# Optimization experiments

Measured on AMD Instinct MI355X. Metric: run time of the kernel, lower is better.

## Reference

```python
import math
import jax, jax.numpy as jnp
import numpy as np

HIDDEN = 1024
INTER = 2048
NUM_EXPERTS = 8          # includes 1 noop slot (last column)
TOP_K = 2
CAPACITY_FACTOR = 1.0
BATCH, SEQ = 4, 4096


def setup_inputs() -> dict:
    key = jax.random.key(0)
    k_x, k_rw, k_ei, k_eo = jax.random.split(key, 4)
    x = jax.random.normal(k_x, (BATCH, SEQ, HIDDEN), dtype=jnp.float32)
    # Router: nn.Linear(hidden, num_experts) with xavier_uniform weight, zero-ish bias
    limit = math.sqrt(6.0 / (HIDDEN + NUM_EXPERTS))
    router_w = jax.random.uniform(k_rw, (NUM_EXPERTS, HIDDEN), dtype=jnp.float32,
                                  minval=-limit, maxval=limit)
    router_b = jnp.zeros((NUM_EXPERTS,), dtype=jnp.float32)
    # Expert params initialized with randn, exactly as in the torch module
    experts_inter = jax.random.normal(k_ei, (NUM_EXPERTS - 1, HIDDEN, INTER), dtype=jnp.float32)
    experts_out = jax.random.normal(k_eo, (NUM_EXPERTS - 1, INTER, HIDDEN), dtype=jnp.float32)
    return {"x": x, "router_w": router_w, "router_b": router_b,
            "experts_inter": experts_inter, "experts_out": experts_out}


def reference(x, router_w, router_b, experts_inter, experts_out):
    B, S, H = x.shape
    E = router_w.shape[0]
    N = B * S
    capacity = math.ceil(N / E * CAPACITY_FACTOR)  # static (shapes are static)

    x_flat = x.reshape(N, H)
    # Router: linear + softmax over experts
    weights = jax.nn.softmax(x_flat @ router_w.T + router_b, axis=-1)   # [N, E]

    # Top-k sparsification: keep top-k weights per token, zero the rest
    vals, idx = jax.lax.top_k(weights, TOP_K)                            # [N, k]
    topk_w = jnp.zeros_like(weights).at[jnp.arange(N)[:, None], idx].set(vals)

    # Last expert column is the no-op (identity) path
    noop_routed = x_flat * topk_w[:, -1:]                                # [N, H]

    expert_w = topk_w[:, :-1]                                            # [N, E-1]
    mask = (expert_w > 0).astype(jnp.int32)                              # [N, E-1]

    # Per-expert: sort tokens by routing mask (descending), take first `capacity`
    sorted_idx = jnp.argsort(-mask, axis=0)[:capacity]                   # [C, E-1], stable
    sorted_mask = jnp.take_along_axis(mask, sorted_idx, axis=0)          # [C, E-1]

    used_idx = (sorted_idx * sorted_mask).reshape(-1)                    # [C*(E-1)]
    toks = x_flat[used_idx] * sorted_mask.reshape(-1)[:, None].astype(x.dtype)
    toks = toks.reshape(capacity, E - 1, H)                              # [C, E-1, H]
    in_w = jnp.take_along_axis(expert_w, sorted_idx, axis=0)             # [C, E-1]

    # Grouped expert FFN: relu(x W1) W2, weighted by routing prob
    h = jax.nn.relu(jnp.einsum('ceh,ehi->cei', toks, experts_inter))     # [C, E-1, I]
    out = jnp.einsum('cei,eih->ceh', h, experts_out) * in_w[..., None]   # [C, E-1, H]

    # Scatter-add combine (masked slots contribute zeros at index 0)
    combined = jnp.zeros_like(x_flat).at[used_idx].add(out.reshape(-1, H))
    combined = combined + noop_routed
    return combined.reshape(B, S, H)
```

## Files before the change

### kernel.cpp

```cpp
#include <hip/hip_runtime.h>
#include <stdint.h>

#define HIDDEN 1024
#define INTER 2048
#define NEXP 8
#define NE 7
#define NTOK 16384
#define CAP 2048
#define BM 64
#define BN 64
#define BK 64
#define GBM 128
#define GBN 128

typedef __attribute__((ext_vector_type(8))) short short8;
typedef __attribute__((ext_vector_type(4))) float f32x4;

__device__ __forceinline__ unsigned short f2bf(float f) {
  union { float f; unsigned int u; } v;
  v.f = f;
  unsigned int u = v.u;
  unsigned int r = (u + 0x7FFFu + ((u >> 16) & 1u)) >> 16;
  return (unsigned short)r;
}

typedef __attribute__((address_space(1))) const unsigned int gu32;
typedef __attribute__((address_space(3))) unsigned int lu32;
__device__ __forceinline__ void gload16(const void* g, void* l) {
  __builtin_amdgcn_global_load_lds((gu32*)g, (lu32*)l, 16, 0, 0);
}

__global__ __launch_bounds__(256) void prologue_kernel(
    const float* __restrict__ x, const float* __restrict__ rw,
    const float* __restrict__ rb, float* __restrict__ expw,
    float* __restrict__ noopw, unsigned short* __restrict__ xbf,
    float* __restrict__ out) {
  if (blockIdx.x == NTOK / 4) {
    unsigned int* z = (unsigned int*)(xbf + (size_t)NTOK * HIDDEN);
    z[threadIdx.x] = 0u;
    z[threadIdx.x + 256] = 0u;
    return;
  }
  int wid = threadIdx.x >> 6;
  int lane = threadIdx.x & 63;
  int token = blockIdx.x * 4 + wid;
  const float* xr = x + (size_t)token * HIDDEN;
  float4 xv[4];
  float acc[NEXP];
#pragma unroll
  for (int e = 0; e < NEXP; e++) acc[e] = 0.f;
#pragma unroll
  for (int j = 0; j < 4; j++) {
    xv[j] = *(const float4*)(xr + j * 256 + lane * 4);
#pragma unroll
    for (int e = 0; e < NEXP; e++) {
      float4 wv = *(const float4*)(rw + e * HIDDEN + j * 256 + lane * 4);
      acc[e] = fmaf(xv[j].x, wv.x, acc[e]);
      acc[e] = fmaf(xv[j].y, wv.y, acc[e]);
      acc[e] = fmaf(xv[j].z, wv.z, acc[e]);
      acc[e] = fmaf(xv[j].w, wv.w, acc[e]);
    }
  }
#pragma unroll
  for (int e = 0; e < NEXP; e++) {
    float a = acc[e];
#pragma unroll
    for (int off = 32; off > 0; off >>= 1) a += __shfl_xor(a, off);
    acc[e] = a + rb[e];
  }
  float nwv = 0.f;
  if (lane == 0) {
    float m = acc[0];
#pragma unroll
    for (int e = 1; e < NEXP; e++) m = fmaxf(m, acc[e]);
    float w[NEXP];
    float s = 0.f;
#pragma unroll
    for (int e = 0; e < NEXP; e++) { w[e] = expf(acc[e] - m); s += w[e]; }
    float inv = 1.f / s;
#pragma unroll
    for (int e = 0; e < NEXP; e++) w[e] *= inv;
    int t1 = 0;
#pragma unroll
    for (int e = 1; e < NEXP; e++) if (w[e] > w[t1]) t1 = e;
    int t2 = (t1 == 0) ? 1 : 0;
#pragma unroll
    for (int e = 0; e < NEXP; e++) if (e != t1 && w[e] > w[t2]) t2 = e;
    nwv = (t1 == NEXP - 1) ? w[t1] : ((t2 == NEXP - 1) ? w[t2] : 0.f);
    noopw[token] = nwv;
#pragma unroll
    for (int e = 0; e < NE; e++) {
      float v = 0.f;
      if (e == t1) v = w[e];
      if (e == t2) v = w[e];
      expw[(size_t)e * NTOK + token] = v;
    }
  }
  float nw = __shfl(nwv, 0);
  float* orow = out + (size_t)token * HIDDEN;
  unsigned short* brow = xbf + (size_t)token * HIDDEN;
#pragma unroll
  for (int j = 0; j < 4; j++) {
    float4 o = xv[j];
    o.x *= nw; o.y *= nw; o.z *= nw; o.w *= nw;
    *(float4*)(orow + j * 256 + lane * 4) = o;
    ushort4 b;
    b.x = f2bf(xv[j].x); b.y = f2bf(xv[j].y);
    b.z = f2bf(xv[j].z); b.w = f2bf(xv[j].w);
    *(ushort4*)(brow + j * 256 + lane * 4) = b;
  }
}

__global__ __launch_bounds__(1024) void assign_par_kernel(
    const float* __restrict__ expw, int* __restrict__ slot_tok,
    float* __restrict__ slot_w) {
  int e = blockIdx.x;
  int tid = threadIdx.x;
  int lane = tid & 63, w = tid >> 6;
  __shared__ int wtot[16];
  const float* we = expw + (size_t)e * NTOK;
  int base = 0;
#pragma unroll 1
  for (int r = 0; r < NTOK / 1024; r++) {
    int t = r * 1024 + tid;
    float wv = we[t];
    bool flag = wv > 0.f;
    unsigned long long mask = __ballot(flag);
    int lp = __popcll(mask & ((1ull << lane) - 1ull));
    if (lane == 0) wtot[w] = __popcll(mask);
    __syncthreads();
    int pre = 0, tot = 0;
#pragma unroll
    for (int i = 0; i < 16; i++) {
      int v = wtot[i];
      pre += (i < w) ? v : 0;
      tot += v;
    }
    int pos = base + pre + lp;
    if (flag && pos < CAP) {
      slot_tok[e * CAP + pos] = t;
      slot_w[e * CAP + pos] = wv;
    }
    base += tot;
    __syncthreads();
    if (base >= CAP) break;
  }
  int cnt = base < CAP ? base : CAP;
  for (int p = cnt + tid; p < CAP; p += 1024) {
    slot_tok[e * CAP + p] = -1;
    slot_w[e * CAP + p] = 0.f;
  }
}

__global__ __launch_bounds__(256) void transpose_bf16_kernel(
    const float* __restrict__ in, unsigned short* __restrict__ outp,
    int K, int N) {
  int e = blockIdx.z;
  const float* src = in + (size_t)e * K * N;
  unsigned short* dst = outp + (size_t)e * K * N;
  int k0 = blockIdx.y * 64;
  int n0 = blockIdx.x * 64;
  __shared__ float tile[64][65];
  int tid = threadIdx.x;
  int nr = tid & 15;
  int kr = tid >> 4;
#pragma unroll
  for (int i = 0; i < 4; i++) {
    int k = i * 16 + kr;
    float4 v = *(const float4*)(src + (size_t)(k0 + k) * N + n0 + nr * 4);
    tile[k][nr * 4 + 0] = v.x;
    tile[k][nr * 4 + 1] = v.y;
    tile[k][nr * 4 + 2] = v.z;
    tile[k][nr * 4 + 3] = v.w;
  }
  __syncthreads();
  int g = tid & 7;
  int nb = tid >> 3;
#pragma unroll
  for (int i = 0; i < 2; i++) {
    int n = i * 32 + nb;
    short8 p;
#pragma unroll
    for (int j = 0; j < 8; j++) p[j] = (short)f2bf(tile[g * 8 + j][n]);
    *(short8*)(dst + (size_t)(n0 + n) * K + k0 + g * 8) = p;
  }
}

__global__ __launch_bounds__(256) void gemm1_mfma_kernel(
    const unsigned short* __restrict__ xbf, const unsigned short* __restrict__ wiT,
    const int* __restrict__ slot_tok, unsigned short* __restrict__ h) {
  int orig = blockIdx.x + (blockIdx.y << 4) + (blockIdx.z << 8);
  int swz = (orig & 7) * 224 + (orig >> 3);
  int bxi = swz & 15, byi = (swz >> 4) & 15, bzi = swz >> 8;
  int e = bzi;
  const unsigned short* be = wiT + (size_t)e * HIDDEN * INTER;
  unsigned short* he = h + (size_t)e * CAP * INTER;
  int bm0 = byi * GBM;
  int bn0 = bxi * GBN;
  __shared__ __align__(16) unsigned short As[GBM * 64];
  __shared__ __align__(16) unsigned short Bs[GBN * 64];
  int tid = threadIdx.x;
  int lane = tid & 63, w = tid >> 6;
  int wm = w >> 1, wn = w & 1;

  const unsigned short* aptr[4];
  const unsigned short* bptr[4];
#pragma unroll
  for (int c = 0; c < 4; c++) {
    int s = w * 4 + c;
    int r = s * 8 + (lane >> 3);
    int gb = lane & 7;
    int g = gb ^ (r & 7);
    int tok = slot_tok[e * CAP + bm0 + r];
    int row = tok < 0 ? NTOK : tok;
    aptr[c] = xbf + (size_t)row * HIDDEN + g * 8;
    bptr[c] = be + (size_t)(bn0 + r) * HIDDEN + g * 8;
  }

  f32x4 acc[4][4];
#pragma unroll
  for (int i = 0; i < 4; i++)
#pragma unroll
    for (int j = 0; j < 4; j++) acc[i][j] = (f32x4){0.f, 0.f, 0.f, 0.f};

  for (int k0 = 0; k0 < HIDDEN; k0 += 64) {
#pragma unroll
    for (int c = 0; c < 4; c++) gload16(aptr[c] + k0, &As[(w * 4 + c) * 512]);
#pragma unroll
    for (int c = 0; c < 4; c++) gload16(bptr[c] + k0, &Bs[(w * 4 + c) * 512]);
    __syncthreads();
#pragma unroll
    for (int kk = 0; kk < 2; kk++) {
      short8 a[4], b[4];
#pragma unroll
      for (int fm = 0; fm < 4; fm++) {
        int r = wm * 64 + fm * 16 + (lane & 15);
        int gb = (kk * 4 + (lane >> 4)) ^ (r & 7);
        a[fm] = *(const short8*)&As[r * 64 + gb * 8];
      }
#pragma unroll
      for (int fn = 0; fn < 4; fn++) {
        int n = wn * 64 + fn * 16 + (lane & 15);
        int gb = (kk * 4 + (lane >> 4)) ^ (n & 7);
        b[fn] = *(const short8*)&Bs[n * 64 + gb * 8];
      }
#pragma unroll
      for (int fm = 0; fm < 4; fm++)
#pragma unroll
        for (int fn = 0; fn < 4; fn++)
          acc[fm][fn] = __builtin_amdgcn_mfma_f32_16x16x32_bf16(
              a[fm], b[fn], acc[fm][fn], 0, 0, 0);
    }
    __syncthreads();
  }
#pragma unroll
  for (int fm = 0; fm < 4; fm++)
#pragma unroll
    for (int r4 = 0; r4 < 4; r4++) {
      int m = bm0 + wm * 64 + fm * 16 + ((lane >> 4) << 2) + r4;
#pragma unroll
      for (int fn = 0; fn < 4; fn++) {
        int n = bn0 + wn * 64 + fn * 16 + (lane & 15);
        float v = acc[fm][fn][r4];
        he[(size_t)m * INTER + n] = f2bf(v > 0.f ? v : 0.f);
      }
    }
}

__global__ __launch_bounds__(256) void gemm2_mfma_kernel(
    const unsigned short* __restrict__ h, const unsigned short* __restrict__ woT,
    const int* __restrict__ slot_tok, const float* __restrict__ slot_w,
    float* __restrict__ out) {
  int orig = blockIdx.x + (blockIdx.y << 3) + (blockIdx.z << 7);
  int swz = (orig & 7) * 112 + (orig >> 3);
  int bxi = swz & 7, byi = (swz >> 3) & 15, bzi = swz >> 7;
  int e = bzi;
  const unsigned short* ae = h + (size_t)e * CAP * INTER;
  const unsigned short* be = woT + (size_t)e * INTER * HIDDEN;
  int bm0 = byi * GBM;
  int bn0 = bxi * GBN;
  __shared__ __align__(16) unsigned short As[GBM * 64];
  __shared__ __align__(16) unsigned short Bs[GBN * 64];
  int tid = threadIdx.x;
  int lane = tid & 63, w = tid >> 6;
  int wm = w >> 1, wn = w & 1;

  const unsigned short* aptr[4];
  const unsigned short* bptr[4];
#pragma unroll
  for (int c = 0; c < 4; c++) {
    int s = w * 4 + c;
    int r = s * 8 + (lane >> 3);
    int gb = lane & 7;
    int g = gb ^ (r & 7);
    aptr[c] = ae + (size_t)(bm0 + r) * INTER + g * 8;
    bptr[c] = be + (size_t)(bn0 + r) * INTER + g * 8;
  }

  f32x4 acc[4][4];
#pragma unroll
  for (int i = 0; i < 4; i++)
#pragma unroll
    for (int j = 0; j < 4; j++) acc[i][j] = (f32x4){0.f, 0.f, 0.f, 0.f};

  for (int k0 = 0; k0 < INTER; k0 += 64) {
#pragma unroll
    for (int c = 0; c < 4; c++) gload16(aptr[c] + k0, &As[(w * 4 + c) * 512]);
#pragma unroll
    for (int c = 0; c < 4; c++) gload16(bptr[c] + k0, &Bs[(w * 4 + c) * 512]);
    __syncthreads();
#pragma unroll
    for (int kk = 0; kk < 2; kk++) {
      short8 a[4], b[4];
#pragma unroll
      for (int fm = 0; fm < 4; fm++) {
        int r = wm * 64 + fm * 16 + (lane & 15);
        int gb = (kk * 4 + (lane >> 4)) ^ (r & 7);
        a[fm] = *(const short8*)&As[r * 64 + gb * 8];
      }
#pragma unroll
      for (int fn = 0; fn < 4; fn++) {
        int n = wn * 64 + fn * 16 + (lane & 15);
        int gb = (kk * 4 + (lane >> 4)) ^ (n & 7);
        b[fn] = *(const short8*)&Bs[n * 64 + gb * 8];
      }
#pragma unroll
      for (int fm = 0; fm < 4; fm++)
#pragma unroll
        for (int fn = 0; fn < 4; fn++)
          acc[fm][fn] = __builtin_amdgcn_mfma_f32_16x16x32_bf16(
              a[fm], b[fn], acc[fm][fn], 0, 0, 0);
    }
    __syncthreads();
  }
#pragma unroll
  for (int fm = 0; fm < 4; fm++)
#pragma unroll
    for (int r4 = 0; r4 < 4; r4++) {
      int m = bm0 + wm * 64 + fm * 16 + ((lane >> 4) << 2) + r4;
      int tok = slot_tok[e * CAP + m];
      float sw = slot_w[e * CAP + m];
      if (tok >= 0) {
#pragma unroll
        for (int fn = 0; fn < 4; fn++) {
          int n = bn0 + wn * 64 + fn * 16 + (lane & 15);
          unsafeAtomicAdd(out + (size_t)tok * HIDDEN + n, acc[fm][fn][r4] * sw);
        }
      }
    }
}

__global__ __launch_bounds__(256) void router_kernel(
    const float* __restrict__ x, const float* __restrict__ rw,
    const float* __restrict__ rb, float* __restrict__ expw,
    float* __restrict__ noopw) {
  int wid = threadIdx.x >> 6;
  int lane = threadIdx.x & 63;
  int token = blockIdx.x * 4 + wid;
  const float* xr = x + (size_t)token * HIDDEN;
  float acc[NEXP];
#pragma unroll
  for (int e = 0; e < NEXP; e++) acc[e] = 0.f;
#pragma unroll
  for (int j = 0; j < HIDDEN / 64; j++) {
    int k = j * 64 + lane;
    float xv = xr[k];
#pragma unroll
    for (int e = 0; e < NEXP; e++) acc[e] = fmaf(xv, rw[e * HIDDEN + k], acc[e]);
  }
#pragma unroll
  for (int e = 0; e < NEXP; e++) {
    float a = acc[e];
#pragma unroll
    for (int off = 32; off > 0; off >>= 1) a += __shfl_xor(a, off);
    acc[e] = a + rb[e];
  }
  if (lane == 0) {
    float m = acc[0];
#pragma unroll
    for (int e = 1; e < NEXP; e++) m = fmaxf(m, acc[e]);
    float w[NEXP];
    float s = 0.f;
#pragma unroll
    for (int e = 0; e < NEXP; e++) { w[e] = expf(acc[e] - m); s += w[e]; }
    float inv = 1.f / s;
#pragma unroll
    for (int e = 0; e < NEXP; e++) w[e] *= inv;
    int t1 = 0;
#pragma unroll
    for (int e = 1; e < NEXP; e++) if (w[e] > w[t1]) t1 = e;
    int t2 = (t1 == 0) ? 1 : 0;
#pragma unroll
    for (int e = 0; e < NEXP; e++) if (e != t1 && w[e] > w[t2]) t2 = e;
    noopw[token] = (t1 == NEXP - 1) ? w[t1] : ((t2 == NEXP - 1) ? w[t2] : 0.f);
#pragma unroll
    for (int e = 0; e < NE; e++) {
      float v = 0.f;
      if (e == t1) v = w[e];
      if (e == t2) v = w[e];
      expw[(size_t)e * NTOK + token] = v;
    }
  }
}

__global__ void assign_kernel(const float* __restrict__ expw,
                              int* __restrict__ slot_tok,
                              float* __restrict__ slot_w) {
  int e = blockIdx.x;
  int lane = threadIdx.x;
  const float* we = expw + (size_t)e * NTOK;
  int base = 0;
  for (int t0 = 0; t0 < NTOK; t0 += 64) {
    float w = we[t0 + lane];
    bool flag = w > 0.f;
    unsigned long long mask = __ballot(flag);
    int prefix = __popcll(mask & ((1ull << lane) - 1ull));
    int pos = base + prefix;
    if (flag && pos < CAP) {
      slot_tok[e * CAP + pos] = t0 + lane;
      slot_w[e * CAP + pos] = w;
    }
    base += __popcll(mask);
    if (base >= CAP) break;
  }
  int cnt = base < CAP ? base : CAP;
  for (int p = cnt + lane; p < CAP; p += 64) {
    slot_tok[e * CAP + p] = -1;
    slot_w[e * CAP + p] = 0.f;
  }
}

__global__ __launch_bounds__(256) void noop_kernel(
    const float* __restrict__ x, const float* __restrict__ noopw,
    float* __restrict__ out) {
  size_t i = (size_t)blockIdx.x * 256 + threadIdx.x;
  float4 v = ((const float4*)x)[i];
  float w = noopw[i >> 8];
  v.x *= w; v.y *= w; v.z *= w; v.w *= w;
  ((float4*)out)[i] = v;
}

__global__ __launch_bounds__(256) void gemm1_kernel(
    const float* __restrict__ x, const float* __restrict__ wi,
    const int* __restrict__ slot_tok, unsigned short* __restrict__ h,
    int e_base) {
  int e = e_base + blockIdx.z;
  unsigned short* he = h + (size_t)blockIdx.z * ((size_t)CAP * INTER);
  const float* wie = wi + (size_t)e * HIDDEN * INTER;
  int bm0 = blockIdx.y * BM;
  int bn0 = blockIdx.x * BN;
  __shared__ __align__(16) unsigned short As[BM][BK];
  __shared__ __align__(16) unsigned short Bs[BN][BK];
  int tid = threadIdx.x;
  int lane = tid & 63;
  int wid = tid >> 6;
  int wm = wid >> 1, wn = wid & 1;
  int tokA[2];
#pragma unroll
  for (int t = 0; t < 2; t++)
    tokA[t] = slot_tok[e * CAP + bm0 + ((tid + t * 256) >> 3)];
  f32x4 acc[2][2];
#pragma unroll
  for (int i = 0; i < 2; i++)
#pragma unroll
    for (int j = 0; j < 2; j++) acc[i][j] = (f32x4){0.f, 0.f, 0.f, 0.f};
  for (int k0 = 0; k0 < HIDDEN; k0 += BK) {
#pragma unroll
    for (int t = 0; t < 2; t++) {
      int idx = tid + t * 256;
      int r = idx >> 3, g = idx & 7;
      short8 pack;
      if (tokA[t] >= 0) {
        const float* src = x + (size_t)tokA[t] * HIDDEN + k0 + g * 8;
        float4 v0 = ((const float4*)src)[0];
        float4 v1 = ((const float4*)src)[1];
        pack[0] = (short)f2bf(v0.x); pack[1] = (short)f2bf(v0.y);
        pack[2] = (short)f2bf(v0.z); pack[3] = (short)f2bf(v0.w);
        pack[4] = (short)f2bf(v1.x); pack[5] = (short)f2bf(v1.y);
        pack[6] = (short)f2bf(v1.z); pack[7] = (short)f2bf(v1.w);
      } else {
        pack = (short8){0, 0, 0, 0, 0, 0, 0, 0};
      }
      int gs = g ^ (r & 7);
      *(short8*)(&As[r][gs * 8]) = pack;
    }
#pragma unroll
    for (int t = 0; t < 2; t++) {
      int idx = tid + t * 256;
      int k = idx >> 3, g = idx & 7;
      const float* src = wie + (size_t)(k0 + k) * INTER + bn0 + g * 8;
      float4 v0 = ((const float4*)src)[0];
      float4 v1 = ((const float4*)src)[1];
      float f[8] = {v0.x, v0.y, v0.z, v0.w, v1.x, v1.y, v1.z, v1.w};
#pragma unroll
      for (int i2 = 0; i2 < 8; i2++) {
        int n = g * 8 + i2;
        int kc = k ^ ((n & 7) << 3);
        Bs[n][kc] = f2bf(f[i2]);
      }
    }
    __syncthreads();
#pragma unroll
    for (int kk = 0; kk < 2; kk++) {
      short8 a[2], b[2];
#pragma unroll
      for (int fm = 0; fm < 2; fm++) {
        int r = wm * 32 + fm * 16 + (lane & 15);
        int gs = (kk * 4 + (lane >> 4)) ^ (r & 7);
        a[fm] = *(const short8*)(&As[r][gs * 8]);
      }
#pragma unroll
      for (int fn = 0; fn < 2; fn++) {
        int n = wn * 32 + fn * 16 + (lane & 15);
        int gs = (kk * 4 + (lane >> 4)) ^ (n & 7);
        b[fn] = *(const short8*)(&Bs[n][gs * 8]);
      }
#pragma unroll
      for (int fm = 0; fm < 2; fm++)
#pragma unroll
        for (int fn = 0; fn < 2; fn++)
          acc[fm][fn] = __builtin_amdgcn_mfma_f32_16x16x32_bf16(
              a[fm], b[fn], acc[fm][fn], 0, 0, 0);
    }
    __syncthreads();
  }
#pragma unroll
  for (int fm = 0; fm < 2; fm++)
#pragma unroll
    for (int fn = 0; fn < 2; fn++)
#pragma unroll
      for (int r = 0; r < 4; r++) {
        int m = bm0 + wm * 32 + fm * 16 + ((lane >> 4) << 2) + r;
        int n = bn0 + wn * 32 + fn * 16 + (lane & 15);
        float v = acc[fm][fn][r];
        v = v > 0.f ? v : 0.f;
        he[(size_t)m * INTER + n] = f2bf(v);
      }
}

__global__ __launch_bounds__(256) void gemm2_kernel(
    const unsigned short* __restrict__ h, const float* __restrict__ wo,
    const int* __restrict__ slot_tok, const float* __restrict__ slot_w,
    float* __restrict__ out, int e_base) {
  int e = e_base + blockIdx.z;
  const unsigned short* he = h + (size_t)blockIdx.z * ((size_t)CAP * INTER);
  const float* woe = wo + (size_t)e * INTER * HIDDEN;
  int bm0 = blockIdx.y * BM;
  int bn0 = blockIdx.x * BN;
  __shared__ __align__(16) unsigned short As[BM][BK];
  __shared__ __align__(16) unsigned short Bs[BN][BK];
  int tid = threadIdx.x;
  int lane = tid & 63;
  int wid = tid >> 6;
  int wm = wid >> 1, wn = wid & 1;
  f32x4 acc[2][2];
#pragma unroll
  for (int i = 0; i < 2; i++)
#pragma unroll
    for (int j = 0; j < 2; j++) acc[i][j] = (f32x4){0.f, 0.f, 0.f, 0.f};
  for (int k0 = 0; k0 < INTER; k0 += BK) {
#pragma unroll
    for (int t = 0; t < 2; t++) {
      int idx = tid + t * 256;
      int r = idx >> 3, g = idx & 7;
      short8 pack = *(const short8*)(he + (size_t)(bm0 + r) * INTER + k0 + g * 8);
      int gs = g ^ (r & 7);
      *(short8*)(&As[r][gs * 8]) = pack;
    }
#pragma unroll
    for (int t = 0; t < 2; t++) {
      int idx = tid + t * 256;
      int k = idx >> 3, g = idx & 7;
      const float* src = woe + (size_t)(k0 + k) * HIDDEN + bn0 + g * 8;
      float4 v0 = ((const float4*)src)[0];
      float4 v1 = ((const float4*)src)[1];
      float f[8] = {v0.x, v0.y, v0.z, v0.w, v1.x, v1.y, v1.z, v1.w};
#pragma unroll
      for (int i2 = 0; i2 < 8; i2++) {
        int n = g * 8 + i2;
        int kc = k ^ ((n & 7) << 3);
        Bs[n][kc] = f2bf(f[i2]);
      }
    }
    __syncthreads();
#pragma unroll
    for (int kk = 0; kk < 2; kk++) {
      short8 a[2], b[2];
#pragma unroll
      for (int fm = 0; fm < 2; fm++) {
        int r = wm * 32 + fm * 16 + (lane & 15);
        int gs = (kk * 4 + (lane >> 4)) ^ (r & 7);
        a[fm] = *(const short8*)(&As[r][gs * 8]);
      }
#pragma unroll
      for (int fn = 0; fn < 2; fn++) {
        int n = wn * 32 + fn * 16 + (lane & 15);
        int gs = (kk * 4 + (lane >> 4)) ^ (n & 7);
        b[fn] = *(const short8*)(&Bs[n][gs * 8]);
      }
#pragma unroll
      for (int fm = 0; fm < 2; fm++)
#pragma unroll
        for (int fn = 0; fn < 2; fn++)
          acc[fm][fn] = __builtin_amdgcn_mfma_f32_16x16x32_bf16(
              a[fm], b[fn], acc[fm][fn], 0, 0, 0);
    }
    __syncthreads();
  }
#pragma unroll
  for (int fm = 0; fm < 2; fm++)
#pragma unroll
    for (int r = 0; r < 4; r++) {
      int m = bm0 + wm * 32 + fm * 16 + ((lane >> 4) << 2) + r;
      int tok = slot_tok[e * CAP + m];
      float sw = slot_w[e * CAP + m];
      if (tok >= 0) {
#pragma unroll
        for (int fn = 0; fn < 2; fn++) {
          int n = bn0 + wn * 32 + fn * 16 + (lane & 15);
          unsafeAtomicAdd(out + (size_t)tok * HIDDEN + n, acc[fm][fn][r] * sw);
        }
      }
    }
}

extern "C" void kernel_launch(void* const* d_in, const int* in_sizes, int n_in,
                              void* d_out, int out_size, void* d_ws, size_t ws_size,
                              hipStream_t stream) {
  const float* x = (const float*)d_in[0];
  const float* rw = (const float*)d_in[1];
  const float* rb = (const float*)d_in[2];
  const float* wi = (const float*)d_in[3];
  const float* wo = (const float*)d_in[4];
  float* out = (float*)d_out;
  char* ws = (char*)d_ws;

  const size_t h_bytes = (size_t)NE * CAP * INTER * 2;
  const size_t xbf_bytes = (size_t)(NTOK + 1) * HIDDEN * 2;
  const size_t wT_bytes = (size_t)NE * HIDDEN * INTER * 2;
  const size_t P_bytes = xbf_bytes + wT_bytes;
  const size_t small_bytes = (size_t)NE * NTOK * 4 + (size_t)NTOK * 4 +
                             (size_t)NE * CAP * 4 * 2;
  const size_t need_new = h_bytes + P_bytes + small_bytes;

  if (ws_size >= need_new) {
    unsigned short* h = (unsigned short*)ws;
    char* P = ws + h_bytes;
    unsigned short* xbf = (unsigned short*)P;
    unsigned short* wiT = (unsigned short*)(P + xbf_bytes);
    unsigned short* woT = (unsigned short*)P;
    char* smalls = P + P_bytes;
    float* expw = (float*)smalls;
    float* noopw = expw + (size_t)NE * NTOK;
    int* slot_tok = (int*)(noopw + NTOK);
    float* slot_w = (float*)(slot_tok + (size_t)NE * CAP);

    prologue_kernel<<<NTOK / 4 + 1, 256, 0, stream>>>(x, rw, rb, expw, noopw,
                                                      xbf, out);
    assign_par_kernel<<<NE, 1024, 0, stream>>>(expw, slot_tok, slot_w);
    transpose_bf16_kernel<<<dim3(INTER / 64, HIDDEN / 64, NE), 256, 0, stream>>>(
        wi, wiT, HIDDEN, INTER);
    gemm1_mfma_kernel<<<dim3(INTER / GBN, CAP / GBM, NE), 256, 0, stream>>>(
        xbf, wiT, slot_tok, h);
    transpose_bf16_kernel<<<dim3(HIDDEN / 64, INTER / 64, NE), 256, 0, stream>>>(
        wo, woT, INTER, HIDDEN);
    gemm2_mfma_kernel<<<dim3(HIDDEN / GBN, CAP / GBM, NE), 256, 0, stream>>>(
        h, woT, slot_tok, slot_w, out);
    return;
  }

  const size_t h_full = (size_t)NE * CAP * INTER * 2;
  const size_t h_one = (size_t)CAP * INTER * 2;
  bool full = ws_size >= h_full + small_bytes;
  size_t hb = full ? h_full : h_one;
  unsigned short* h = (unsigned short*)ws;
  float* expw = (float*)(ws + hb);
  float* noopw = expw + (size_t)NE * NTOK;
  int* slot_tok = (int*)(noopw + NTOK);
  float* slot_w = (float*)(slot_tok + (size_t)NE * CAP);

  router_kernel<<<NTOK / 4, 256, 0, stream>>>(x, rw, rb, expw, noopw);
  assign_kernel<<<NE, 64, 0, stream>>>(expw, slot_tok, slot_w);
  noop_kernel<<<(NTOK * (HIDDEN / 4)) / 256, 256, 0, stream>>>(x, noopw, out);
  if (full) {
    gemm1_kernel<<<dim3(INTER / BN, CAP / BM, NE), 256, 0, stream>>>(
        x, wi, slot_tok, h, 0);
    gemm2_kernel<<<dim3(HIDDEN / BN, CAP / BM, NE), 256, 0, stream>>>(
        h, wo, slot_tok, slot_w, out, 0);
  } else {
    for (int e = 0; e < NE; e++) {
      gemm1_kernel<<<dim3(INTER / BN, CAP / BM, 1), 256, 0, stream>>>(
          x, wi, slot_tok, h, e);
      gemm2_kernel<<<dim3(HIDDEN / BN, CAP / BM, 1), 256, 0, stream>>>(
          h, wo, slot_tok, slot_w, out, e);
    }
  }
}
```

Baseline: 430.3 us.

## Double-buffer LDS tiles in expert GEMMs to overlap global loads with MFMA

Both expert GEMM kernels now keep two LDS buffers for the A and B tiles and issue the global-to-LDS loads for the next K slice before computing on the current one. The goal is to hide global memory latency behind MFMA work instead of stalling at a barrier after every load. In exchange, LDS use per block doubles to 64 KB, which may lower occupancy. The direct-to-LDS loads still rely on the barrier placement being correct for the in-flight buffer.

```diff
diff --git a/kernel.cpp b/kernel.cpp
--- a/kernel.cpp
+++ b/kernel.cpp
@@ -197,8 +197,8 @@
   unsigned short* he = h + (size_t)e * CAP * INTER;
   int bm0 = byi * GBM;
   int bn0 = bxi * GBN;
-  __shared__ __align__(16) unsigned short As[GBM * 64];
-  __shared__ __align__(16) unsigned short Bs[GBN * 64];
+  __shared__ __align__(16) unsigned short As[2][GBM * 64];
+  __shared__ __align__(16) unsigned short Bs[2][GBN * 64];
   int tid = threadIdx.x;
   int lane = tid & 63, w = tid >> 6;
   int wm = w >> 1, wn = w & 1;
@@ -223,12 +223,14 @@
 #pragma unroll
     for (int j = 0; j < 4; j++) acc[i][j] = (f32x4){0.f, 0.f, 0.f, 0.f};
 
-  for (int k0 = 0; k0 < HIDDEN; k0 += 64) {
-#pragma unroll
-    for (int c = 0; c < 4; c++) gload16(aptr[c] + k0, &As[(w * 4 + c) * 512]);
-#pragma unroll
-    for (int c = 0; c < 4; c++) gload16(bptr[c] + k0, &Bs[(w * 4 + c) * 512]);
-    __syncthreads();
+  auto stage = [&](int k0, unsigned short* A, unsigned short* B) {
+#pragma unroll
+    for (int c = 0; c < 4; c++) {
+      gload16(aptr[c] + k0, A + (w * 4 + c) * 512);
+      gload16(bptr[c] + k0, B + (w * 4 + c) * 512);
+    }
+  };
+  auto compute = [&](const unsigned short* A, const unsigned short* B) {
 #pragma unroll
     for (int kk = 0; kk < 2; kk++) {
       short8 a[4], b[4];
@@ -236,13 +238,13 @@
       for (int fm = 0; fm < 4; fm++) {
         int r = wm * 64 + fm * 16 + (lane & 15);
         int gb = (kk * 4 + (lane >> 4)) ^ (r & 7);
-        a[fm] = *(const short8*)&As[r * 64 + gb * 8];
+        a[fm] = *(const short8*)&A[r * 64 + gb * 8];
       }
 #pragma unroll
       for (int fn = 0; fn < 4; fn++) {
         int n = wn * 64 + fn * 16 + (lane & 15);
         int gb = (kk * 4 + (lane >> 4)) ^ (n & 7);
-        b[fn] = *(const short8*)&Bs[n * 64 + gb * 8];
+        b[fn] = *(const short8*)&B[n * 64 + gb * 8];
       }
 #pragma unroll
       for (int fm = 0; fm < 4; fm++)
@@ -251,6 +253,17 @@
           acc[fm][fn] = __builtin_amdgcn_mfma_f32_16x16x32_bf16(
               a[fm], b[fn], acc[fm][fn], 0, 0, 0);
     }
+  };
+
+  stage(0, As[0], Bs[0]);
+  __syncthreads();
+#pragma unroll 1
+  for (int k0 = 0; k0 < HIDDEN; k0 += 128) {
+    stage(k0 + 64, As[1], Bs[1]);
+    compute(As[0], Bs[0]);
+    __syncthreads();
+    if (k0 + 128 < HIDDEN) stage(k0 + 128, As[0], Bs[0]);
+    compute(As[1], Bs[1]);
     __syncthreads();
   }
 #pragma unroll
@@ -279,8 +292,8 @@
   const unsigned short* be = woT + (size_t)e * INTER * HIDDEN;
   int bm0 = byi * GBM;
   int bn0 = bxi * GBN;
-  __shared__ __align__(16) unsigned short As[GBM * 64];
-  __shared__ __align__(16) unsigned short Bs[GBN * 64];
+  __shared__ __align__(16) unsigned short As[2][GBM * 64];
+  __shared__ __align__(16) unsigned short Bs[2][GBN * 64];
   int tid = threadIdx.x;
   int lane = tid & 63, w = tid >> 6;
   int wm = w >> 1, wn = w & 1;
@@ -303,12 +316,14 @@
 #pragma unroll
     for (int j = 0; j < 4; j++) acc[i][j] = (f32x4){0.f, 0.f, 0.f, 0.f};
 
-  for (int k0 = 0; k0 < INTER; k0 += 64) {
-#pragma unroll
-    for (int c = 0; c < 4; c++) gload16(aptr[c] + k0, &As[(w * 4 + c) * 512]);
-#pragma unroll
-    for (int c = 0; c < 4; c++) gload16(bptr[c] + k0, &Bs[(w * 4 + c) * 512]);
-    __syncthreads();
+  auto stage = [&](int k0, unsigned short* A, unsigned short* B) {
+#pragma unroll
+    for (int c = 0; c < 4; c++) {
+      gload16(aptr[c] + k0, A + (w * 4 + c) * 512);
+      gload16(bptr[c] + k0, B + (w * 4 + c) * 512);
+    }
+  };
+  auto compute = [&](const unsigned short* A, const unsigned short* B) {
 #pragma unroll
     for (int kk = 0; kk < 2; kk++) {
       short8 a[4], b[4];
@@ -316,13 +331,13 @@
       for (int fm = 0; fm < 4; fm++) {
         int r = wm * 64 + fm * 16 + (lane & 15);
         int gb = (kk * 4 + (lane >> 4)) ^ (r & 7);
-        a[fm] = *(const short8*)&As[r * 64 + gb * 8];
+        a[fm] = *(const short8*)&A[r * 64 + gb * 8];
       }
 #pragma unroll
       for (int fn = 0; fn < 4; fn++) {
         int n = wn * 64 + fn * 16 + (lane & 15);
         int gb = (kk * 4 + (lane >> 4)) ^ (n & 7);
-        b[fn] = *(const short8*)&Bs[n * 64 + gb * 8];
+        b[fn] = *(const short8*)&B[n * 64 + gb * 8];
       }
 #pragma unroll
       for (int fm = 0; fm < 4; fm++)
@@ -331,6 +346,17 @@
           acc[fm][fn] = __builtin_amdgcn_mfma_f32_16x16x32_bf16(
               a[fm], b[fn], acc[fm][fn], 0, 0, 0);
     }
+  };
+
+  stage(0, As[0], Bs[0]);
+  __syncthreads();
+#pragma unroll 1
+  for (int k0 = 0; k0 < INTER; k0 += 128) {
+    stage(k0 + 64, As[1], Bs[1]);
+    compute(As[0], Bs[0]);
+    __syncthreads();
+    if (k0 + 128 < INTER) stage(k0 + 128, As[0], Bs[0]);
+    compute(As[1], Bs[1]);
     __syncthreads();
   }
 #pragma unroll
```

Measured after the change: 450.7 us. +4.7%, slower.
